# Optimization experiments

Hardware: AMD Instinct MI355X
Metric: run time of the kernel (lower is better)

## Reference

```python
import jax, jax.numpy as jnp
import numpy as np

B, NQ, NK = 4, 2048, 2048
D_MODEL, H, DK, DV, M = 512, 8, 64, 64, 40


def setup_inputs() -> dict:
    key = jax.random.key(0)
    ks = jax.random.split(key, 12)
    s = 0.02  # param init scale (stand-in for xavier)
    return {
        "queries": jax.random.normal(ks[0], (B, NQ, D_MODEL), jnp.float32),
        "keys": jax.random.normal(ks[1], (B, NK, D_MODEL), jnp.float32),
        "values": jax.random.normal(ks[2], (B, NK, D_MODEL), jnp.float32),
        "attention_weights": jax.random.uniform(ks[3], (B, H, NQ, NK), jnp.float32),
        "attention_mask": jax.random.randint(ks[4], (B, H, NQ, NK), 0, 2) == 1,
        "Wq": jax.random.normal(ks[5], (D_MODEL, H * DK), jnp.float32) * s,
        "bq": jnp.zeros((H * DK,), jnp.float32),
        "Wk": jax.random.normal(ks[6], (D_MODEL, H * DK), jnp.float32) * s,
        "bk": jnp.zeros((H * DK,), jnp.float32),
        "Wv": jax.random.normal(ks[7], (D_MODEL, H * DV), jnp.float32) * s,
        "bv": jnp.zeros((H * DV,), jnp.float32),
        "Wo": jax.random.normal(ks[8], (H * DV, D_MODEL), jnp.float32) * s,
        "bo": jnp.zeros((D_MODEL,), jnp.float32),
        "m_k": jax.random.normal(ks[9], (1, M, H * DK), jnp.float32) * s,
        "m_v": jax.random.normal(ks[10], (1, M, H * DV), jnp.float32) * s,
    }


def reference(queries, keys, values, attention_weights, attention_mask,
              Wq, bq, Wk, bk, Wv, bv, Wo, bo, m_k, m_v):
    b, nq, _ = queries.shape
    nk = keys.shape[1]
    # learned memory slots, scaled and broadcast over batch
    mk = jnp.sqrt(jnp.float32(DK)) * jnp.broadcast_to(m_k, (b, M, H * DK))
    mv = jnp.sqrt(jnp.float32(M)) * jnp.broadcast_to(m_v, (b, M, H * DV))
    q = (queries @ Wq + bq).reshape(b, nq, H, DK).transpose(0, 2, 1, 3)      # (b,h,nq,dk)
    k = jnp.concatenate([keys @ Wk + bk, mk], axis=1)
    k = k.reshape(b, nk + M, H, DK).transpose(0, 2, 3, 1)                     # (b,h,dk,nk+m)
    v = jnp.concatenate([values @ Wv + bv, mv], axis=1)
    v = v.reshape(b, nk + M, H, DV).transpose(0, 2, 1, 3)                     # (b,h,nk+m,dv)
    att = jnp.matmul(q, k) / jnp.sqrt(jnp.float32(DK))                        # (b,h,nq,nk+m)
    att_x = att[..., :nk] * attention_weights
    att_x = jnp.where(attention_mask, -jnp.inf, att_x)
    att = jnp.concatenate([att_x, att[..., nk:]], axis=-1)
    att = jax.nn.softmax(att, axis=-1)
    out = jnp.matmul(att, v).transpose(0, 2, 1, 3).reshape(b, nq, H * DV)
    return out @ Wo + bo
```

## Files before the change

kernel.cpp:

```cpp
#include <hip/hip_runtime.h>
#include <hip/hip_bf16.h>
#include <cstdint>
#include <cstddef>

typedef __bf16 bf16_t;
typedef __bf16 bf16x8 __attribute__((ext_vector_type(8)));
typedef __bf16 bf16x4 __attribute__((ext_vector_type(4)));
typedef float  f32x4  __attribute__((ext_vector_type(4)));

#define B_    4
#define NQ_   2048
#define NK_   2048
#define H_    8
#define MSL_  40
#define NKP_  2112
#define SCL2  0.18033688011112042f

#define GLOAD_LDS16(GP, LP)                                                        \
    __builtin_amdgcn_global_load_lds(                                              \
        (const __attribute__((address_space(1))) unsigned int*)(GP),               \
        (__attribute__((address_space(3))) unsigned int*)(LP), 16, 0, 0)

__global__ void detect_mask(const unsigned int* __restrict__ m, int* __restrict__ flag)
{
    __shared__ int found;
    if (threadIdx.x == 0) found = 0;
    __syncthreads();
    unsigned int acc = 0;
    for (int i = threadIdx.x; i < 65536; i += 256)
        acc |= (m[i] & 0xFFFFFF00u);
    if (acc) found = 1;
    __syncthreads();
    if (threadIdx.x == 0) *flag = found;
}

__global__ void transpose_convert4(const float* __restrict__ s0, const float* __restrict__ s1,
                                   const float* __restrict__ s2, const float* __restrict__ s3,
                                   bf16_t* __restrict__ d0, bf16_t* __restrict__ d1,
                                   bf16_t* __restrict__ d2, bf16_t* __restrict__ d3)
{
    const float* src; bf16_t* dst;
    switch (blockIdx.z) {
        case 0:  src = s0; dst = d0; break;
        case 1:  src = s1; dst = d1; break;
        case 2:  src = s2; dst = d2; break;
        default: src = s3; dst = d3; break;
    }
    __shared__ float t[32][33];
    int x  = blockIdx.x * 32 + threadIdx.x;
    int y0 = blockIdx.y * 32 + threadIdx.y;
#pragma unroll
    for (int i = 0; i < 32; i += 8)
        t[threadIdx.y + i][threadIdx.x] = src[(size_t)(y0 + i) * 512 + x];
    __syncthreads();
    int ox  = blockIdx.y * 32 + threadIdx.x;
    int oy0 = blockIdx.x * 32 + threadIdx.y;
#pragma unroll
    for (int i = 0; i < 32; i += 8)
        dst[(size_t)(oy0 + i) * 512 + ox] = (bf16_t)t[threadIdx.x][threadIdx.y + i];
}

__global__ void memfill(const float* __restrict__ m_k, const float* __restrict__ m_v,
                        bf16_t* __restrict__ Kbf, bf16_t* __restrict__ Vt)
{
    int tid = blockIdx.x * 256 + threadIdx.x;
    if (tid < 4 * 64 * 512) {
        int c  = tid & 511;
        int mi = (tid >> 9) & 63;
        int b  = tid >> 15;
        float v = (mi < MSL_) ? 8.0f * m_k[mi * 512 + c] : 0.0f;
        Kbf[((size_t)b * NKP_ + NK_ + mi) * 512 + c] = (bf16_t)v;
    } else {
        int t  = tid - 4 * 64 * 512;
        int mi = t & 63;
        int dv = (t >> 6) & 63;
        int h  = (t >> 12) & 7;
        int b  = t >> 15;
        float v = (mi < MSL_) ? 6.324555320336759f * m_v[mi * 512 + h * 64 + dv] : 0.0f;
        Vt[(((size_t)b * H_ + h) * 64 + dv) * NKP_ + NK_ + mi] = (bf16_t)v;
    }
}

template<bool AF32>
__device__ __forceinline__ void gemm_core(
    bf16_t (*As)[72], bf16_t (*Bs)[72],
    const void* __restrict__ Av, const bf16_t* __restrict__ BT,
    const float* __restrict__ bias, void* __restrict__ dstv,
    int dstBS, int epi, float scale)
{
    const int tid = threadIdx.x;
    const int w = tid >> 6, l = tid & 63, lg = l >> 4, lr = l & 15;
    const int wr = w >> 1, wc = w & 1;
    const int blockM = blockIdx.x * 128, blockN = blockIdx.y * 128;

    f32x4 acc[4][4];
    const f32x4 zv = {0.f, 0.f, 0.f, 0.f};
#pragma unroll
    for (int i = 0; i < 4; i++)
#pragma unroll
        for (int j = 0; j < 4; j++) acc[i][j] = zv;

    const int ar = tid >> 1;
    const int ac = (tid & 1) * 32;

    for (int k0 = 0; k0 < 512; k0 += 64) {
        if (k0) __syncthreads();
        if constexpr (AF32) {
            const float* arow = (const float*)Av + (size_t)(blockM + ar) * 512 + k0 + ac;
#pragma unroll
            for (int i = 0; i < 8; i++) {
                float4 v = ((const float4*)arow)[i];
                bf16x4 pk = {(bf16_t)v.x, (bf16_t)v.y, (bf16_t)v.z, (bf16_t)v.w};
                *(bf16x4*)&As[ar][ac + i * 4] = pk;
            }
        } else {
            const bf16_t* arow = (const bf16_t*)Av + (size_t)(blockM + ar) * 512 + k0 + ac;
#pragma unroll
            for (int i = 0; i < 4; i++)
                *(uint4*)&As[ar][ac + i * 8] = ((const uint4*)arow)[i];
        }
        {
            const bf16_t* brow = BT + (size_t)(blockN + ar) * 512 + k0 + ac;
#pragma unroll
            for (int i = 0; i < 4; i++)
                *(uint4*)&Bs[ar][ac + i * 8] = ((const uint4*)brow)[i];
        }
        __syncthreads();
#pragma unroll
        for (int ks = 0; ks < 2; ks++) {
            bf16x8 af[4], bfr[4];
#pragma unroll
            for (int mi = 0; mi < 4; mi++)
                af[mi] = *(const bf16x8*)&As[wr * 64 + mi * 16 + lr][ks * 32 + lg * 8];
#pragma unroll
            for (int ni = 0; ni < 4; ni++)
                bfr[ni] = *(const bf16x8*)&Bs[wc * 64 + ni * 16 + lr][ks * 32 + lg * 8];
#pragma unroll
            for (int mi = 0; mi < 4; mi++)
#pragma unroll
                for (int ni = 0; ni < 4; ni++)
                    acc[mi][ni] = __builtin_amdgcn_mfma_f32_16x16x32_bf16(af[mi], bfr[ni], acc[mi][ni], 0, 0, 0);
        }
    }

    const int colbase = blockN + wc * 64;
    float bias_v[4];
#pragma unroll
    for (int ni = 0; ni < 4; ni++) bias_v[ni] = bias[colbase + ni * 16 + lr];

#pragma unroll
    for (int mi = 0; mi < 4; mi++) {
        const int r0 = blockM + wr * 64 + mi * 16 + lg * 4;
#pragma unroll
        for (int ni = 0; ni < 4; ni++) {
            const int c = colbase + ni * 16 + lr;
            f32x4 v = acc[mi][ni];
            if (epi == 2) {
                float* dst = (float*)dstv;
#pragma unroll
                for (int j = 0; j < 4; j++)
                    dst[(size_t)(r0 + j) * 512 + c] = (v[j] + bias_v[ni]) * scale;
            } else if (epi == 0) {
                bf16_t* dst = (bf16_t*)dstv;
#pragma unroll
                for (int j = 0; j < 4; j++) {
                    int rr = r0 + j;
                    int bb = rr >> 11, nn = rr & 2047;
                    dst[((size_t)bb * dstBS + nn) * 512 + c] = (bf16_t)((v[j] + bias_v[ni]) * scale);
                }
            } else {
                bf16_t* dst = (bf16_t*)dstv;
                int bb = r0 >> 11, n0 = r0 & 2047;
                int hh = c >> 6, dv = c & 63;
                bf16x4 pk;
#pragma unroll
                for (int j = 0; j < 4; j++) pk[j] = (bf16_t)((v[j] + bias_v[ni]) * scale);
                *(bf16x4*)(dst + (((size_t)bb * H_ + hh) * 64 + dv) * NKP_ + n0) = pk;
            }
        }
    }
}

__global__ __launch_bounds__(256) void gemm_qkv(
    const float* __restrict__ q, const float* __restrict__ k, const float* __restrict__ v,
    const bf16_t* __restrict__ WqT, const bf16_t* __restrict__ WkT, const bf16_t* __restrict__ WvT,
    const float* __restrict__ bq, const float* __restrict__ bk, const float* __restrict__ bv,
    bf16_t* __restrict__ Qbf, bf16_t* __restrict__ Kbf, bf16_t* __restrict__ Vt)
{
    __shared__ bf16_t As[128][72];
    __shared__ bf16_t Bs[128][72];
    const void* Av; const bf16_t* BT; const float* bias; void* dst;
    int dstBS, epi; float scale = 1.0f;
    switch (blockIdx.z) {
        case 0:  Av = q; BT = WqT; bias = bq; dst = Qbf; dstBS = 2048; epi = 0; scale = SCL2; break;
        case 1:  Av = k; BT = WkT; bias = bk; dst = Kbf; dstBS = NKP_; epi = 0; break;
        default: Av = v; BT = WvT; bias = bv; dst = Vt;  dstBS = 0;    epi = 1; break;
    }
    gemm_core<true>(As, Bs, Av, BT, bias, dst, dstBS, epi, scale);
}

__global__ __launch_bounds__(256) void gemm_fin(
    const bf16_t* __restrict__ Obuf, const bf16_t* __restrict__ WoT,
    const float* __restrict__ bo, float* __restrict__ out)
{
    __shared__ bf16_t As[128][72];
    __shared__ bf16_t Bs[128][72];
    gemm_core<false>(As, Bs, Obuf, WoT, bo, out, 0, 2, 1.0f);
}

template<bool BYTEM>
__global__ __launch_bounds__(512) void attn_fused(
    const bf16_t* __restrict__ Qbf, const bf16_t* __restrict__ Kbf,
    const bf16_t* __restrict__ Vt, const float* __restrict__ attw,
    const void* __restrict__ maskv, const int* __restrict__ mflag,
    bf16_t* __restrict__ Obuf)
{
    if ((*mflag != 0) != BYTEM) return;

    __shared__ bf16_t Ks[4][64][64];
    __shared__ bf16_t Vs[4][64][64];
    __shared__ bf16_t Pl[8][1024];

    const int tid = threadIdx.x;
    const int wv = tid >> 6, l = tid & 63, lg = l >> 4, lr = l & 15;
    const int qt = blockIdx.x, h = blockIdx.y, b = blockIdx.z;
    const int q0w = qt * 128 + wv * 16;
    bf16_t* Pw = &Pl[wv][0];

    const size_t bh = (size_t)(b * H_ + h);
    const float* wbase = attw + bh * (size_t)NQ_ * NK_;
    const unsigned char* mb8 = (const unsigned char*)maskv + bh * (size_t)NQ_ * NK_;
    const int* mb32 = (const int*)maskv + bh * (size_t)NQ_ * NK_;
    const char* kbase8 = (const char*)(Kbf + (size_t)b * NKP_ * 512 + h * 64);
    const char* vbase8 = (const char*)(Vt + bh * 64 * (size_t)NKP_);

    bf16x8 qf0 = *(const bf16x8*)&Qbf[((size_t)b * NQ_ + q0w + lr) * 512 + h * 64 + lg * 8];
    bf16x8 qf1 = *(const bf16x8*)&Qbf[((size_t)b * NQ_ + q0w + lr) * 512 + h * 64 + 32 + lg * 8];

    const f32x4 zv = {0.f, 0.f, 0.f, 0.f};
    f32x4 oacc[4];
#pragma unroll
    for (int i = 0; i < 4; i++) oacc[i] = zv;
    float lsum = 0.f;
    f32x4 sA[4];

    f32x4 wA[4], wB[4];
    unsigned mA[4], mB[4];
    unsigned miA[16], miB[16];

    const int srow = l >> 3;
    const int scsw = ((l & 7) ^ (srow & 7)) * 16;

#define STAGE(BUF, KCB) do {                                                      \
    const int r_ = wv * 8 + srow;                                                 \
    GLOAD_LDS16(kbase8 + (size_t)((KCB) + r_) * 1024 + scsw,                      \
                (char*)&Ks[BUF][0][0] + wv * 1024);                               \
    GLOAD_LDS16(vbase8 + (size_t)r_ * 4224 + (size_t)(KCB) * 2 + scsw,            \
                (char*)&Vs[BUF][0][0] + wv * 1024);                               \
} while (0)

#define PREFETCH(KT, WB_, MB_, MIB_) do {                                         \
    const float* wp_ = wbase + (size_t)(q0w + lr) * NK_ + (KT) * 64 + lg * 4;     \
    _Pragma("unroll") for (int n_ = 0; n_ < 4; n_++)                              \
        WB_[n_] = *(const f32x4*)(wp_ + n_ * 16);                                 \
    if constexpr (BYTEM) {                                                        \
        const unsigned char* mp_ = mb8 + (size_t)(q0w + lr) * NK_ + (KT) * 64 + lg * 4; \
        _Pragma("unroll") for (int n_ = 0; n_ < 4; n_++)                          \
            MB_[n_] = *(const unsigned*)(mp_ + n_ * 16);                          \
    } else {                                                                      \
        const int* mp_ = mb32 + (size_t)(q0w + lr) * NK_ + (KT) * 64 + lg * 4;    \
        _Pragma("unroll") for (int n_ = 0; n_ < 4; n_++) {                        \
            uint4 t_ = *(const uint4*)(mp_ + n_ * 16);                            \
            MIB_[n_ * 4 + 0] = t_.x; MIB_[n_ * 4 + 1] = t_.y;                     \
            MIB_[n_ * 4 + 2] = t_.z; MIB_[n_ * 4 + 3] = t_.w; }                   \
    }                                                                             \
} while (0)

#define QKT_LDS(BC) do {                                                          \
    const int sw_ = (lg ^ (lr & 7)) * 8;                                          \
    _Pragma("unroll") for (int n_ = 0; n_ < 4; n_++) {                            \
        const int kr_ = n_ * 16 + lr;                                             \
        f32x4 a_ = zv;                                                            \
        a_ = __builtin_amdgcn_mfma_f32_16x16x32_bf16(*(const bf16x8*)&Ks[BC][kr_][sw_], qf0, a_, 0, 0, 0); \
        a_ = __builtin_amdgcn_mfma_f32_16x16x32_bf16(*(const bf16x8*)&Ks[BC][kr_][sw_ ^ 32], qf1, a_, 0, 0, 0); \
        sA[n_] = a_;                                                              \
    }                                                                             \
} while (0)

#define APPLY(WB_, MB_, MIB_) do {                                                \
    _Pragma("unroll") for (int n_ = 0; n_ < 4; n_++)                              \
    _Pragma("unroll") for (int j_ = 0; j_ < 4; j_++) {                            \
        bool mk_;                                                                 \
        if constexpr (BYTEM) mk_ = ((MB_[n_] >> (8 * j_)) & 0xffu) != 0;          \
        else                 mk_ = (MIB_[n_ * 4 + j_] != 0);                      \
        sA[n_][j_] = mk_ ? -1e30f : sA[n_][j_] * WB_[n_][j_];                     \
    }                                                                             \
} while (0)

#define SMPV(BC) do {                                                             \
    _Pragma("unroll") for (int n_ = 0; n_ < 4; n_++)                              \
    _Pragma("unroll") for (int j_ = 0; j_ < 4; j_++) {                            \
        float p_ = exp2f(sA[n_][j_]);                                             \
        sA[n_][j_] = p_; lsum += p_;                                              \
    }                                                                             \
    _Pragma("unroll") for (int n_ = 0; n_ < 4; n_++) {                            \
        int c_ = n_ * 2 + (lg >> 1);                                              \
        int qp_ = (lr + 4 * c_) & 15;                                             \
        bf16x4 pk_ = {(bf16_t)sA[n_][0], (bf16_t)sA[n_][1],                       \
                      (bf16_t)sA[n_][2], (bf16_t)sA[n_][3]};                      \
        *(bf16x4*)&Pw[c_ * 128 + qp_ * 8 + (lg & 1) * 4] = pk_;                   \
    }                                                                             \
    bf16x8 pf0_ = *(const bf16x8*)&Pw[lg * 128 + ((lr + 4 * lg) & 15) * 8];       \
    bf16x8 pf1_ = *(const bf16x8*)&Pw[(4 + lg) * 128 + ((lr + 4 * (4 + lg)) & 15) * 8]; \
    const int vsw_ = (lg ^ (lr & 7)) * 8;                                         \
    _Pragma("unroll") for (int n2_ = 0; n2_ < 4; n2_++) {                         \
        const int vr_ = n2_ * 16 + lr;                                            \
        oacc[n2_] = __builtin_amdgcn_mfma_f32_16x16x32_bf16(*(const bf16x8*)&Vs[BC][vr_][vsw_], pf0_, oacc[n2_], 0, 0, 0); \
        oacc[n2_] = __builtin_amdgcn_mfma_f32_16x16x32_bf16(*(const bf16x8*)&Vs[BC][vr_][vsw_ ^ 32], pf1_, oacc[n2_], 0, 0, 0); \
    }                                                                             \
} while (0)

#define SUBB(T, BC, W_, M_, MI_) do {                                            \
    QKT_LDS(BC);                                                                  \
    APPLY(W_, M_, MI_);                                                           \
    if ((T) < 30) PREFETCH((T) + 2, W_, M_, MI_);                                 \
    SMPV(BC);                                                                     \
} while (0)

#define PERIOD(T, B0, B1, S0, S1) do {                                            \
    if ((T) + 2 < 32) STAGE(S0, ((T) + 2) * 64);                                  \
    if ((T) + 3 < 32) STAGE(S1, ((T) + 3) * 64);                                  \
    SUBB((T),     B0, wA, mA, miA);                                               \
    SUBB((T) + 1, B1, wB, mB, miB);                                               \
    __syncthreads();                                                              \
} while (0)

    STAGE(0, 2048);
    STAGE(1, 0);
    STAGE(2, 64);
    PREFETCH(0, wA, mA, miA);
    __syncthreads();

    {
        QKT_LDS(0);
#pragma unroll
        for (int n_ = 0; n_ < 4; n_++)
#pragma unroll
            for (int j_ = 0; j_ < 4; j_++) {
                int kloc = n_ * 16 + lg * 4 + j_;
                sA[n_][j_] = (kloc >= MSL_) ? -1e30f : sA[n_][j_];
            }
        PREFETCH(1, wB, mB, miB);
        SMPV(0);
        __syncthreads();
    }

    for (int t = 0; t < 28; t += 4) {
        PERIOD(t,     1, 2, 3, 0);
        PERIOD(t + 2, 3, 0, 1, 2);
    }
    PERIOD(28, 1, 2, 3, 0);
    SUBB(30, 3, wA, mA, miA);
    SUBB(31, 0, wB, mB, miB);

    float ts = lsum;
    ts += __shfl_xor(ts, 16);
    ts += __shfl_xor(ts, 32);
    float invl = 1.0f / ts;
#pragma unroll
    for (int n2 = 0; n2 < 4; n2++) {
        bf16x4 ov = {(bf16_t)(oacc[n2][0] * invl), (bf16_t)(oacc[n2][1] * invl),
                     (bf16_t)(oacc[n2][2] * invl), (bf16_t)(oacc[n2][3] * invl)};
        *(bf16x4*)&Obuf[((size_t)b * NQ_ + q0w + lr) * 512 + h * 64 + n2 * 16 + lg * 4] = ov;
    }

#undef STAGE
#undef PREFETCH
#undef QKT_LDS
#undef APPLY
#undef SMPV
#undef SUBB
#undef PERIOD
}

extern "C" void kernel_launch(void* const* d_in, const int* in_sizes, int n_in,
                              void* d_out, int out_size, void* d_ws, size_t ws_size,
                              hipStream_t stream)
{
    const float* queries = (const float*)d_in[0];
    const float* keys    = (const float*)d_in[1];
    const float* values  = (const float*)d_in[2];
    const float* attw    = (const float*)d_in[3];
    const void*  maskv   = d_in[4];
    const float* Wq = (const float*)d_in[5];
    const float* bq = (const float*)d_in[6];
    const float* Wk = (const float*)d_in[7];
    const float* bk = (const float*)d_in[8];
    const float* Wv = (const float*)d_in[9];
    const float* bv = (const float*)d_in[10];
    const float* Wo = (const float*)d_in[11];
    const float* bo = (const float*)d_in[12];
    const float* m_k = (const float*)d_in[13];
    const float* m_v = (const float*)d_in[14];

    char* ws = (char*)d_ws;
    bf16_t* WqT  = (bf16_t*)(ws + 0);
    bf16_t* WkT  = (bf16_t*)(ws + 524288);
    bf16_t* WvT  = (bf16_t*)(ws + 1048576);
    bf16_t* WoT  = (bf16_t*)(ws + 1572864);
    bf16_t* Qbf  = (bf16_t*)(ws + 2097152);
    bf16_t* Kbf  = (bf16_t*)(ws + 10485760);
    bf16_t* Vt   = (bf16_t*)(ws + 19136512);
    bf16_t* Obuf = (bf16_t*)(ws + 27787264);
    int*    mflag = (int*)(ws + 36175872);

    detect_mask<<<1, 256, 0, stream>>>((const unsigned int*)maskv, mflag);
    transpose_convert4<<<dim3(16, 16, 4), dim3(32, 8), 0, stream>>>(
        Wq, Wk, Wv, Wo, WqT, WkT, WvT, WoT);
    memfill<<<1024, 256, 0, stream>>>(m_k, m_v, Kbf, Vt);

    gemm_qkv<<<dim3(64, 4, 3), 256, 0, stream>>>(
        queries, keys, values, WqT, WkT, WvT, bq, bk, bv, Qbf, Kbf, Vt);

    attn_fused<true><<<dim3(16, H_, B_), 512, 0, stream>>>(Qbf, Kbf, Vt, attw, maskv, mflag, Obuf);
    attn_fused<false><<<dim3(16, H_, B_), 512, 0, stream>>>(Qbf, Kbf, Vt, attw, maskv, mflag, Obuf);

    gemm_fin<<<dim3(64, 4), 256, 0, stream>>>(Obuf, WoT, bo, (float*)d_out);
    (void)in_sizes; (void)n_in; (void)out_size; (void)ws_size;
}
```

Measured before the change: 336.5 us.

## Triple-buffer attention-weight and mask register prefetch to deepen load lookahead

Adds a third register buffer set for the per-tile attention weights and mask and rotates the three sets across periods. Each tile's weights and mask are now fetched earlier relative to their use, so more HBM latency for the large weight and mask streams is hidden behind the QK/softmax/PV work. The steady-state loop is unrolled into a six-period rotation. The cost is higher VGPR pressure from the extra buffers, which may lower occupancy or cause spills.

```diff
diff --git a/kernel.cpp b/kernel.cpp
--- a/kernel.cpp
+++ b/kernel.cpp
@@ -244,9 +244,9 @@
     float lsum = 0.f;
     f32x4 sA[4];
 
-    f32x4 wA[4], wB[4];
-    unsigned mA[4], mB[4];
-    unsigned miA[16], miB[16];
+    f32x4 wA[4], wB[4], wC[4];
+    unsigned mA[4], mB[4], mC[4];
+    unsigned miA[16], miB[16], miC[16];
 
     const int srow = l >> 3;
     const int scsw = ((l & 7) ^ (srow & 7)) * 16;
@@ -320,18 +320,19 @@
     }                                                                             \
 } while (0)
 
-#define SUBB(T, BC, W_, M_, MI_) do {                                            \
-    QKT_LDS(BC);                                                                  \
-    APPLY(W_, M_, MI_);                                                           \
-    if ((T) < 30) PREFETCH((T) + 2, W_, M_, MI_);                                 \
-    SMPV(BC);                                                                     \
-} while (0)
-
-#define PERIOD(T, B0, B1, S0, S1) do {                                            \
-    if ((T) + 2 < 32) STAGE(S0, ((T) + 2) * 64);                                  \
-    if ((T) + 3 < 32) STAGE(S1, ((T) + 3) * 64);                                  \
-    SUBB((T),     B0, wA, mA, miA);                                               \
-    SUBB((T) + 1, B1, wB, mB, miB);                                               \
+#define SUBB(BC, W_, M_, MI_) do {                                                \
+    QKT_LDS(BC); APPLY(W_, M_, MI_); SMPV(BC);                                    \
+} while (0)
+
+#define PERIOD(T, B0, B1, S0, S1, C0,MC0,MIC0, C1,MC1,MIC1, SP,MSP,MISP) do {     \
+    STAGE(S0, ((T) + 2) * 64);                                                    \
+    STAGE(S1, ((T) + 3) * 64);                                                    \
+    PREFETCH((T) + 2, SP, MSP, MISP);                                             \
+    QKT_LDS(B0);                                                                  \
+    APPLY(C0, MC0, MIC0);                                                         \
+    PREFETCH((T) + 3, C0, MC0, MIC0);                                             \
+    SMPV(B0);                                                                     \
+    SUBB(B1, C1, MC1, MIC1);                                                      \
     __syncthreads();                                                              \
 } while (0)
 
@@ -339,6 +340,7 @@
     STAGE(1, 0);
     STAGE(2, 64);
     PREFETCH(0, wA, mA, miA);
+    PREFETCH(1, wB, mB, miB);
     __syncthreads();
 
     {
@@ -350,18 +352,23 @@
                 int kloc = n_ * 16 + lg * 4 + j_;
                 sA[n_][j_] = (kloc >= MSL_) ? -1e30f : sA[n_][j_];
             }
-        PREFETCH(1, wB, mB, miB);
         SMPV(0);
         __syncthreads();
     }
 
-    for (int t = 0; t < 28; t += 4) {
-        PERIOD(t,     1, 2, 3, 0);
-        PERIOD(t + 2, 3, 0, 1, 2);
-    }
-    PERIOD(28, 1, 2, 3, 0);
-    SUBB(30, 3, wA, mA, miA);
-    SUBB(31, 0, wB, mB, miB);
+    for (int t = 0; t < 24; t += 12) {
+        PERIOD(t,      1, 2, 3, 0,  wA,mA,miA, wB,mB,miB, wC,mC,miC);
+        PERIOD(t + 2,  3, 0, 1, 2,  wC,mC,miC, wA,mA,miA, wB,mB,miB);
+        PERIOD(t + 4,  1, 2, 3, 0,  wB,mB,miB, wC,mC,miC, wA,mA,miA);
+        PERIOD(t + 6,  3, 0, 1, 2,  wA,mA,miA, wB,mB,miB, wC,mC,miC);
+        PERIOD(t + 8,  1, 2, 3, 0,  wC,mC,miC, wA,mA,miA, wB,mB,miB);
+        PERIOD(t + 10, 3, 0, 1, 2,  wB,mB,miB, wC,mC,miC, wA,mA,miA);
+    }
+    PERIOD(24, 1, 2, 3, 0,  wA,mA,miA, wB,mB,miB, wC,mC,miC);
+    PERIOD(26, 3, 0, 1, 2,  wC,mC,miC, wA,mA,miA, wB,mB,miB);
+    PERIOD(28, 1, 2, 3, 0,  wB,mB,miB, wC,mC,miC, wA,mA,miA);
+    SUBB(3, wA, mA, miA);
+    SUBB(0, wB, mB, miB);
 
     float ts = lsum;
     ts += __shfl_xor(ts, 16);
```

Result: slower. 345.6 us (+2.7%).

## Double-buffer LDS tiles in projection GEMMs with register prefetch

Applied to the files above, without the earlier changes.

The shared GEMM core used by the QKV projection and output projection now keeps two LDS buffers for the A and B tiles. It prefetches the next K-slice from global memory into registers while MFMAs run on the current buffer, then writes those registers into the other buffer. This removes one barrier per iteration and hides global load latency behind compute. In exchange it doubles LDS use per block (about 73KB) and raises register pressure from the prefetch registers, which may lower occupancy.

```diff
diff --git a/kernel.cpp b/kernel.cpp
--- a/kernel.cpp
+++ b/kernel.cpp
@@ -83,7 +83,7 @@
 
 template<bool AF32>
 __device__ __forceinline__ void gemm_core(
-    bf16_t (*As)[72], bf16_t (*Bs)[72],
+    bf16_t (*As)[128][72], bf16_t (*Bs)[128][72],
     const void* __restrict__ Av, const bf16_t* __restrict__ BT,
     const float* __restrict__ bias, void* __restrict__ dstv,
     int dstBS, int epi, float scale)
@@ -103,45 +103,67 @@
     const int ar = tid >> 1;
     const int ac = (tid & 1) * 32;
 
-    for (int k0 = 0; k0 < 512; k0 += 64) {
-        if (k0) __syncthreads();
-        if constexpr (AF32) {
-            const float* arow = (const float*)Av + (size_t)(blockM + ar) * 512 + k0 + ac;
-#pragma unroll
-            for (int i = 0; i < 8; i++) {
-                float4 v = ((const float4*)arow)[i];
-                bf16x4 pk = {(bf16_t)v.x, (bf16_t)v.y, (bf16_t)v.z, (bf16_t)v.w};
-                *(bf16x4*)&As[ar][ac + i * 4] = pk;
-            }
-        } else {
-            const bf16_t* arow = (const bf16_t*)Av + (size_t)(blockM + ar) * 512 + k0 + ac;
-#pragma unroll
-            for (int i = 0; i < 4; i++)
-                *(uint4*)&As[ar][ac + i * 8] = ((const uint4*)arow)[i];
-        }
-        {
-            const bf16_t* brow = BT + (size_t)(blockN + ar) * 512 + k0 + ac;
-#pragma unroll
-            for (int i = 0; i < 4; i++)
-                *(uint4*)&Bs[ar][ac + i * 8] = ((const uint4*)brow)[i];
-        }
+    float4 ra[8];
+    uint4  ra16[4];
+    uint4  rb[4];
+
+#define GLOADT(K0) do {                                                           \
+    if constexpr (AF32) {                                                         \
+        const float* arow_ = (const float*)Av + (size_t)(blockM + ar) * 512 + (K0) + ac; \
+        _Pragma("unroll") for (int i_ = 0; i_ < 8; i_++)                          \
+            ra[i_] = ((const float4*)arow_)[i_];                                  \
+    } else {                                                                      \
+        const bf16_t* arow_ = (const bf16_t*)Av + (size_t)(blockM + ar) * 512 + (K0) + ac; \
+        _Pragma("unroll") for (int i_ = 0; i_ < 4; i_++)                          \
+            ra16[i_] = ((const uint4*)arow_)[i_];                                 \
+    }                                                                             \
+    const bf16_t* brow_ = BT + (size_t)(blockN + ar) * 512 + (K0) + ac;           \
+    _Pragma("unroll") for (int i_ = 0; i_ < 4; i_++)                              \
+        rb[i_] = ((const uint4*)brow_)[i_];                                       \
+} while (0)
+
+#define LDSWRITE(BUF) do {                                                        \
+    if constexpr (AF32) {                                                         \
+        _Pragma("unroll") for (int i_ = 0; i_ < 8; i_++) {                        \
+            float4 v_ = ra[i_];                                                   \
+            bf16x4 pk_ = {(bf16_t)v_.x, (bf16_t)v_.y, (bf16_t)v_.z, (bf16_t)v_.w}; \
+            *(bf16x4*)&As[BUF][ar][ac + i_ * 4] = pk_;                            \
+        }                                                                         \
+    } else {                                                                      \
+        _Pragma("unroll") for (int i_ = 0; i_ < 4; i_++)                          \
+            *(uint4*)&As[BUF][ar][ac + i_ * 8] = ra16[i_];                        \
+    }                                                                             \
+    _Pragma("unroll") for (int i_ = 0; i_ < 4; i_++)                              \
+        *(uint4*)&Bs[BUF][ar][ac + i_ * 8] = rb[i_];                              \
+} while (0)
+
+    GLOADT(0);
+    LDSWRITE(0);
+
+    for (int kk = 0; kk < 8; kk++) {
         __syncthreads();
+        if (kk < 7) GLOADT((kk + 1) * 64);
+        const int cb = kk & 1;
 #pragma unroll
         for (int ks = 0; ks < 2; ks++) {
             bf16x8 af[4], bfr[4];
 #pragma unroll
             for (int mi = 0; mi < 4; mi++)
-                af[mi] = *(const bf16x8*)&As[wr * 64 + mi * 16 + lr][ks * 32 + lg * 8];
+                af[mi] = *(const bf16x8*)&As[cb][wr * 64 + mi * 16 + lr][ks * 32 + lg * 8];
 #pragma unroll
             for (int ni = 0; ni < 4; ni++)
-                bfr[ni] = *(const bf16x8*)&Bs[wc * 64 + ni * 16 + lr][ks * 32 + lg * 8];
+                bfr[ni] = *(const bf16x8*)&Bs[cb][wc * 64 + ni * 16 + lr][ks * 32 + lg * 8];
 #pragma unroll
             for (int mi = 0; mi < 4; mi++)
 #pragma unroll
                 for (int ni = 0; ni < 4; ni++)
                     acc[mi][ni] = __builtin_amdgcn_mfma_f32_16x16x32_bf16(af[mi], bfr[ni], acc[mi][ni], 0, 0, 0);
         }
-    }
+        if (kk < 7) LDSWRITE(cb ^ 1);
+    }
+
+#undef GLOADT
+#undef LDSWRITE
 
     const int colbase = blockN + wc * 64;
     float bias_v[4];
@@ -187,8 +209,8 @@
     const float* __restrict__ bq, const float* __restrict__ bk, const float* __restrict__ bv,
     bf16_t* __restrict__ Qbf, bf16_t* __restrict__ Kbf, bf16_t* __restrict__ Vt)
 {
-    __shared__ bf16_t As[128][72];
-    __shared__ bf16_t Bs[128][72];
+    __shared__ bf16_t As[2][128][72];
+    __shared__ bf16_t Bs[2][128][72];
     const void* Av; const bf16_t* BT; const float* bias; void* dst;
     int dstBS, epi; float scale = 1.0f;
     switch (blockIdx.z) {
@@ -203,8 +225,8 @@
     const bf16_t* __restrict__ Obuf, const bf16_t* __restrict__ WoT,
     const float* __restrict__ bo, float* __restrict__ out)
 {
-    __shared__ bf16_t As[128][72];
-    __shared__ bf16_t Bs[128][72];
+    __shared__ bf16_t As[2][128][72];
+    __shared__ bf16_t Bs[2][128][72];
     gemm_core<false>(As, Bs, Obuf, WoT, bo, out, 0, 2, 1.0f);
 }
 
```

Measured after the change: 334.0 us. Within noise of the previous version (-0.7%).
